# Performance work log

Hardware: AMD Instinct MI355X
Metric: run time of the kernel (lower is better)

## Reference

```python
import jax, jax.numpy as jnp
from jax import lax
import numpy as np

PATCH_H = 8
PATCH_W = 8


def setup_inputs() -> dict:
    key = jax.random.key(0)
    k1, k2 = jax.random.split(key)
    x = jax.random.normal(k1, (2, 1024, 256, 256), dtype=jnp.float32)
    # Conv1d weight [C_out, C_in, k], bias=False
    conv_w = jax.random.normal(k2, (1024, 1024, 3), dtype=jnp.float32) * 0.02
    return {"x": x, "conv_w": conv_w}


def reference(x, conv_w):
    B, C, H, W = x.shape
    hf, wf = H // PATCH_H, W // PATCH_W
    P = hf * wf
    # Patch average pool: mean over each (PATCH_H, PATCH_W) tile -> [B, C, hf, wf]
    xp = x.reshape(B, C, hf, PATCH_H, wf, PATCH_W)
    y = xp.mean(axis=(3, 5)).reshape(B, C, P)
    # Conv1d over the patch axis (SAME padding, no bias), then sigmoid gate
    g = lax.conv_general_dilated(
        y, conv_w, window_strides=(1,), padding="SAME",
        dimension_numbers=("NCH", "OIH", "NCH"))
    g = jax.nn.sigmoid(g).reshape(B, C, hf, wf)
    # Broadcast gate back over each patch and multiply
    out = xp * g[:, :, :, None, :, None]
    return out.reshape(B, C, H, W)
```

## Files before the change

### kernel.cpp

```cpp
#include <hip/hip_runtime.h>
#include <hip/hip_bf16.h>

#define HH 256
#define WW 256
#define CCH 1024
#define NB 2
#define HF 32
#define WF 32
#define PP 1024

using f32x4 = __attribute__((ext_vector_type(4))) float;
using short8 = __attribute__((ext_vector_type(8))) short;

__global__ __launch_bounds__(256) void pool_kernel(const float* __restrict__ x,
                                                   float* __restrict__ y) {
    int blk = blockIdx.x;
    int ph  = blk & 31;
    int bc  = blk >> 5;
    int t   = threadIdx.x;
    const float* xp = x + ((size_t)bc * HH + (size_t)ph * 8) * WW;
    int r    = t >> 6;
    int col4 = (t & 63) * 4;
    float s = 0.f;
#pragma unroll
    for (int it = 0; it < 2; ++it) {
        f32x4 v = __builtin_nontemporal_load(
            (const f32x4*)(xp + (size_t)(r + it * 4) * WW + col4));
        s += v.x + v.y + v.z + v.w;
    }
    __shared__ float red[256];
    red[t] = s;
    __syncthreads();
    if (t < 32) {
        float tot = 0.f;
#pragma unroll
        for (int r4 = 0; r4 < 4; ++r4)
            tot += red[r4 * 64 + 2 * t] + red[r4 * 64 + 2 * t + 1];
        y[(size_t)bc * PP + ph * WF + t] = tot * (1.f / 64.f);
    }
}

__global__ __launch_bounds__(256) void wconv_pad_kernel(const float* __restrict__ w,
                                                        __hip_bfloat16* __restrict__ wT,
                                                        __hip_bfloat16* __restrict__ yT) {
    int tid = blockIdx.x * 256 + threadIdx.x;
    const float* p = w + (size_t)tid * 3;
    float a = p[0], b = p[1], c = p[2];
    wT[tid]               = __float2bfloat16(a);
    wT[(1u << 20) + tid]  = __float2bfloat16(b);
    wT[(2u << 20) + tid]  = __float2bfloat16(c);
    if (tid < 2 * CCH) {
        int bb = tid >> 10, cc = tid & 1023;
        __hip_bfloat16 z = __float2bfloat16(0.f);
        __hip_bfloat16* base = yT + (size_t)bb * (PP + 2) * CCH;
        base[cc] = z;
        base[(size_t)(PP + 1) * CCH + cc] = z;
    }
}

__global__ __launch_bounds__(256) void transpose_kernel(const float* __restrict__ y,
                                                        __hip_bfloat16* __restrict__ yT) {
    int b  = blockIdx.z;
    int c0 = blockIdx.x * 32;
    int p0 = blockIdx.y * 32;
    __shared__ float tile[32][33];
    int tx = threadIdx.x, ty = threadIdx.y;
    const float* yb = y + (size_t)b * CCH * PP;
#pragma unroll
    for (int rr = 0; rr < 4; ++rr)
        tile[ty + rr * 8][tx] = yb[(size_t)(c0 + ty + rr * 8) * PP + p0 + tx];
    __syncthreads();
    __hip_bfloat16* yTb = yT + (size_t)b * (PP + 2) * CCH;
#pragma unroll
    for (int rr = 0; rr < 4; ++rr)
        yTb[(size_t)(1 + p0 + ty + rr * 8) * CCH + c0 + tx] =
            __float2bfloat16(tile[tx][ty + rr * 8]);
}

__global__ __launch_bounds__(256) void conv_gemm_kernel(
        const __hip_bfloat16* __restrict__ wT,
        const __hip_bfloat16* __restrict__ yT,
        float* __restrict__ gate) {
    int lane = threadIdx.x & 63;
    int wid  = threadIdx.x >> 6;
    int l15 = lane & 15, lhi = lane >> 4;
    int co_base = blockIdx.x * 64 + wid * 16;
    int p_base  = blockIdx.y * 32;
    int b = blockIdx.z;
    const __hip_bfloat16* yTb = yT + (size_t)b * (PP + 2) * CCH;

    f32x4 acc[2] = {};
#pragma unroll
    for (int tap = 0; tap < 3; ++tap) {
        const __hip_bfloat16* Ap = wT + (size_t)tap * (1u << 20)
                                 + (size_t)(co_base + l15) * CCH + lhi * 8;
        const __hip_bfloat16* Bp = yTb + (size_t)(p_base + l15 + tap) * CCH + lhi * 8;
        for (int ci0 = 0; ci0 < CCH; ci0 += 32) {
            short8 a0 = *(const short8*)(Ap + ci0);
            short8 b0 = *(const short8*)(Bp + ci0);
            short8 b1 = *(const short8*)(Bp + ci0 + 16 * CCH);
            acc[0] = __builtin_amdgcn_mfma_f32_16x16x32_bf16(a0, b0, acc[0], 0, 0, 0);
            acc[1] = __builtin_amdgcn_mfma_f32_16x16x32_bf16(a0, b1, acc[1], 0, 0, 0);
        }
    }
    float* gb = gate + (size_t)b * CCH * PP;
#pragma unroll
    for (int j16 = 0; j16 < 2; ++j16) {
        int col  = p_base + j16 * 16 + l15;
        int row0 = co_base + lhi * 4;
#pragma unroll
        for (int r = 0; r < 4; ++r) {
            float v = acc[j16][r];
            gb[(size_t)(row0 + r) * PP + col] = 1.f / (1.f + __expf(-v));
        }
    }
}

__global__ __launch_bounds__(256) void apply_kernel(const float* __restrict__ x,
                                                    const float* __restrict__ gate,
                                                    float* __restrict__ out) {
    size_t i0 = (size_t)blockIdx.x * blockDim.x + threadIdx.x;
    size_t stride = (size_t)gridDim.x * blockDim.x;
    const size_t total4 = (size_t)1 << 25;
    for (size_t i4 = i0; i4 < total4; i4 += stride) {
        int w4 = (int)(i4 & 63);
        int h  = (int)((i4 >> 6) & 255);
        int c  = (int)((i4 >> 14) & 1023);
        int b  = (int)(i4 >> 24);
        int p  = (h >> 3) * 32 + (w4 >> 1);
        float g = gate[(((size_t)b * 1024 + c) << 10) + p];
        f32x4 v = __builtin_nontemporal_load((const f32x4*)x + i4);
        v *= g;
        __builtin_nontemporal_store(v, (f32x4*)out + i4);
    }
}

extern "C" void kernel_launch(void* const* d_in, const int* in_sizes, int n_in,
                              void* d_out, int out_size, void* d_ws, size_t ws_size,
                              hipStream_t stream) {
    const float* x = (const float*)d_in[0];
    const float* w = (const float*)d_in[1];
    float* out = (float*)d_out;

    char* ws = (char*)d_ws;
    float*          y    = (float*)(ws);
    __hip_bfloat16* yT   = (__hip_bfloat16*)(ws + 8388608);
    __hip_bfloat16* wT   = (__hip_bfloat16*)(ws + 12591104);
    float*          gate = (float*)(ws + 18882560);

    hipLaunchKernelGGL(pool_kernel,      dim3(65536),      dim3(256),    0, stream, x, y);
    hipLaunchKernelGGL(wconv_pad_kernel, dim3(4096),       dim3(256),    0, stream, w, wT, yT);
    hipLaunchKernelGGL(transpose_kernel, dim3(32, 32, 2),  dim3(32, 8),  0, stream, y, yT);
    hipLaunchKernelGGL(conv_gemm_kernel, dim3(16, 32, 2),  dim3(256),    0, stream, wT, yT, gate);
    hipLaunchKernelGGL(apply_kernel,     dim3(2048),       dim3(256),    0, stream, x, gate, out);
}
```

Before: 426.5 us.

## Restructure pool, conv GEMM and apply kernels around per-channel blocks

The pool kernel now uses one block per (batch, channel) plane. Each wavefront sums 8-row slabs and combines pairs with a shuffle, which removes the shared-memory reduction and the barrier. The conv GEMM block grows to 512 threads covering 64 patches, so each weight row is shared by two waves. The apply kernel processes one channel plane per block and stages that channel's 1024 gate values in LDS, replacing the scattered per-element global gate loads and the index arithmetic. The trade-off is fewer, larger blocks, which may lower parallelism for the memory-bound pool and apply passes.

Result: no change. 427.2 us (+0.2%).

```diff
diff --git a/kernel.cpp b/kernel.cpp
--- a/kernel.cpp
+++ b/kernel.cpp
@@ -4,9 +4,6 @@
 #define HH 256
 #define WW 256
 #define CCH 1024
-#define NB 2
-#define HF 32
-#define WF 32
 #define PP 1024
 
 using f32x4 = __attribute__((ext_vector_type(4))) float;
@@ -14,29 +11,24 @@
 
 __global__ __launch_bounds__(256) void pool_kernel(const float* __restrict__ x,
                                                    float* __restrict__ y) {
-    int blk = blockIdx.x;
-    int ph  = blk & 31;
-    int bc  = blk >> 5;
-    int t   = threadIdx.x;
-    const float* xp = x + ((size_t)bc * HH + (size_t)ph * 8) * WW;
-    int r    = t >> 6;
-    int col4 = (t & 63) * 4;
-    float s = 0.f;
+    int bc   = blockIdx.x;
+    int wid  = threadIdx.x >> 6;
+    int lane = threadIdx.x & 63;
+    const float* xp = x + (size_t)bc * (HH * WW) + lane * 4;
+    float* yp = y + (size_t)bc * PP;
 #pragma unroll
-    for (int it = 0; it < 2; ++it) {
-        f32x4 v = __builtin_nontemporal_load(
-            (const f32x4*)(xp + (size_t)(r + it * 4) * WW + col4));
-        s += v.x + v.y + v.z + v.w;
-    }
-    __shared__ float red[256];
-    red[t] = s;
-    __syncthreads();
-    if (t < 32) {
-        float tot = 0.f;
+    for (int s = 0; s < 8; ++s) {
+        int ph = wid + s * 4;
+        const float* slab = xp + (size_t)ph * 8 * WW;
+        float acc = 0.f;
 #pragma unroll
-        for (int r4 = 0; r4 < 4; ++r4)
-            tot += red[r4 * 64 + 2 * t] + red[r4 * 64 + 2 * t + 1];
-        y[(size_t)bc * PP + ph * WF + t] = tot * (1.f / 64.f);
+        for (int r = 0; r < 8; ++r) {
+            f32x4 v = __builtin_nontemporal_load((const f32x4*)(slab + (size_t)r * WW));
+            acc += v.x + v.y + v.z + v.w;
+        }
+        acc += __shfl_xor(acc, 1);
+        if ((lane & 1) == 0)
+            yp[ph * 32 + (lane >> 1)] = acc * (1.f / 64.f);
     }
 }
 
@@ -77,15 +69,16 @@
             __float2bfloat16(tile[tx][ty + rr * 8]);
 }
 
-__global__ __launch_bounds__(256) void conv_gemm_kernel(
+__global__ __launch_bounds__(512) void conv_gemm_kernel(
         const __hip_bfloat16* __restrict__ wT,
         const __hip_bfloat16* __restrict__ yT,
         float* __restrict__ gate) {
     int lane = threadIdx.x & 63;
     int wid  = threadIdx.x >> 6;
+    int wp  = wid & 1, wco = wid >> 1;
     int l15 = lane & 15, lhi = lane >> 4;
-    int co_base = blockIdx.x * 64 + wid * 16;
-    int p_base  = blockIdx.y * 32;
+    int co_base = blockIdx.x * 64 + wco * 16;
+    int p_base  = blockIdx.y * 64 + wp * 32;
     int b = blockIdx.z;
     const __hip_bfloat16* yTb = yT + (size_t)b * (PP + 2) * CCH;
 
@@ -119,19 +112,24 @@
 __global__ __launch_bounds__(256) void apply_kernel(const float* __restrict__ x,
                                                     const float* __restrict__ gate,
                                                     float* __restrict__ out) {
-    size_t i0 = (size_t)blockIdx.x * blockDim.x + threadIdx.x;
-    size_t stride = (size_t)gridDim.x * blockDim.x;
-    const size_t total4 = (size_t)1 << 25;
-    for (size_t i4 = i0; i4 < total4; i4 += stride) {
-        int w4 = (int)(i4 & 63);
-        int h  = (int)((i4 >> 6) & 255);
-        int c  = (int)((i4 >> 14) & 1023);
-        int b  = (int)(i4 >> 24);
-        int p  = (h >> 3) * 32 + (w4 >> 1);
-        float g = gate[(((size_t)b * 1024 + c) << 10) + p];
-        f32x4 v = __builtin_nontemporal_load((const f32x4*)x + i4);
-        v *= g;
-        __builtin_nontemporal_store(v, (f32x4*)out + i4);
+    int bc = blockIdx.x;
+    const float* xp = x   + (size_t)bc * (HH * WW);
+    float*       op = out + (size_t)bc * (HH * WW);
+    __shared__ float g[PP];
+    int t = threadIdx.x;
+    ((f32x4*)g)[t] = ((const f32x4*)(gate + (size_t)bc * PP))[t];
+    __syncthreads();
+    int col4 = t & 63;
+    int r    = t >> 6;
+    int pc   = col4 >> 1;
+#pragma unroll 4
+    for (int it = 0; it < 64; ++it) {
+        int row = it * 4 + r;
+        float gg = g[(row >> 3) * 32 + pc];
+        size_t off = (size_t)row * 64 + col4;
+        f32x4 v = __builtin_nontemporal_load((const f32x4*)xp + off);
+        v *= gg;
+        __builtin_nontemporal_store(v, (f32x4*)op + off);
     }
 }
 
@@ -148,9 +146,9 @@
     __hip_bfloat16* wT   = (__hip_bfloat16*)(ws + 12591104);
     float*          gate = (float*)(ws + 18882560);
 
-    hipLaunchKernelGGL(pool_kernel,      dim3(65536),      dim3(256),    0, stream, x, y);
-    hipLaunchKernelGGL(wconv_pad_kernel, dim3(4096),       dim3(256),    0, stream, w, wT, yT);
-    hipLaunchKernelGGL(transpose_kernel, dim3(32, 32, 2),  dim3(32, 8),  0, stream, y, yT);
-    hipLaunchKernelGGL(conv_gemm_kernel, dim3(16, 32, 2),  dim3(256),    0, stream, wT, yT, gate);
-    hipLaunchKernelGGL(apply_kernel,     dim3(2048),       dim3(256),    0, stream, x, gate, out);
+    hipLaunchKernelGGL(pool_kernel,      dim3(2048),      dim3(256),   0, stream, x, y);
+    hipLaunchKernelGGL(wconv_pad_kernel, dim3(4096),      dim3(256),   0, stream, w, wT, yT);
+    hipLaunchKernelGGL(transpose_kernel, dim3(32, 32, 2), dim3(32, 8), 0, stream, y, yT);
+    hipLaunchKernelGGL(conv_gemm_kernel, dim3(16, 16, 2), dim3(512),   0, stream, wT, yT, gate);
+    hipLaunchKernelGGL(apply_kernel,     dim3(2048),      dim3(256),   0, stream, x, gate, out);
 }
```
